# Kernel optimization log

Measured on AMD Instinct MI355X. Metric: run time of the kernel, lower is better.

## Reference

```python
import jax, jax.numpy as jnp
import numpy as np

B, S, P, H, W, TAG, M, K = 4, 2, 17, 128, 128, 1, 8, 10
PHW = P * H * W
SIGMA, SF = 0.2, 3.0
E_INV = float(np.e ** -1)
EPS = 1e-6


def setup_inputs() -> dict:
    key = jax.random.key(0)
    k1, k2, k3, k4, k5, k6, k7 = jax.random.split(key, 7)
    preds = jax.random.normal(k1, (B, S, (1 + TAG) * P, H, W), jnp.float32)
    gt_masks = jax.random.uniform(k2, (B, H, W), jnp.float32)
    gt_heatmaps = jax.random.uniform(k3, (B, P, H, W), jnp.float32)
    pos = jax.random.uniform(k4, (B, M, P, 2), jnp.float32) * H  # pixel coords
    vis = jax.random.randint(k5, (B, M, P, 1), 0, 2).astype(jnp.float32)
    gt_skeletons = jnp.concatenate([pos, vis], axis=-1)  # [B,M,P,3] = (x, y, vis)
    kp_idx = jax.random.randint(k6, (B, M, P, 1), 0, PHW)
    kp_vis = jax.random.randint(k7, (B, M, P, 1), 0, 2)
    gt_keypoints = jnp.concatenate([kp_idx, kp_vis], axis=-1).astype(jnp.int32)  # [B,M,J,2]
    return {"preds": preds, "gt_masks": gt_masks, "gt_heatmaps": gt_heatmaps,
            "gt_skeletons": gt_skeletons, "gt_keypoints": gt_keypoints}


def _clog(x):
    # torch BCE clamps log at -100
    return jnp.clip(jnp.log(x), -100.0, None)


def _tag_single(pt, kp):
    # pt: [TAG, PHW] tag map for one (image, stack); kp: [M, J, 2] int (flat_idx, vis)
    idx = kp[..., 0]
    vis = (kp[..., 1] > 0).astype(pt.dtype)  # [M, J]
    g = jnp.transpose(pt[:, idx], (1, 2, 0))  # [M, J, TAG]
    cnt = vis.sum(1)  # [M]
    valid = (cnt > 0).astype(pt.dtype)
    safe = jnp.maximum(cnt, 1.0)
    mean_tag = (g * vis[..., None]).sum(1) / safe[:, None]  # [M, TAG]
    # pull: per-person mean over (visible joints x tag dims) of squared deviation
    pull_pp = (((g - mean_tag[:, None]) ** 2) * vis[..., None]).sum((1, 2)) / (safe * TAG)
    num = valid.sum()
    pull = (pull_pp * valid).sum() / (num + EPS)
    d = ((mean_tag[:, None] - mean_tag[None]) ** 2).sum(-1)  # [M, M]
    pm = jnp.exp(-d) * valid[:, None] * valid[None]
    push = (pm.sum() - num) / ((num - 1.0) * num + EPS) * 0.5
    return push, pull


def _forward(preds, gt_masks, gt_heatmaps, gt_skeletons, gt_keypoints):
    hm = preds[:, :, :P]  # [B,S,P,H,W] raw heatmap logits
    prob = jax.nn.sigmoid(hm)
    # ---- detection loss (weighted BCE, per stack) ----
    t = (gt_heatmaps > E_INV).astype(jnp.float32)[:, None]  # [B,1,P,H,W]
    wgt = 10.0 * t + 0.5 * (gt_heatmaps < E_INV).astype(jnp.float32)[:, None]
    x = prob * gt_masks[:, None, None]
    bce = -(t * _clog(x) + (1.0 - t) * _clog(1.0 - x))
    det_loss = (wgt * bce).mean(axis=(0, 2, 3, 4))  # [S]
    # ---- associative embedding push/pull ----
    pred_tag_imgs = preds[:, :, P:(1 + TAG) * P].reshape(B, S, TAG, P, H, W)
    pred_tags = pred_tag_imgs.reshape(B, S, TAG, PHW)
    push, pull = jax.vmap(lambda ptb, kpb: jax.vmap(lambda pt: _tag_single(pt, kpb))(ptb))(
        pred_tags, gt_keypoints)  # each [B,S]
    # ---- keypoint sampling: top-K of flattened probability maps ----
    flat = prob.reshape(B, S, PHW)
    _, topi = jax.lax.top_k(flat, K)  # [B,S,K]
    part = topi // (H * W)
    rem = topi % (H * W)
    xi = rem // W
    yi = rem % W
    pos = jnp.stack([xi, yi], -1).astype(jnp.float32)  # [B,S,K,2]
    # ---- nearest-person matching (faithful to source, incl. vis==1 penalty) ----
    max_dist = float(H + W)
    sk_t = jnp.transpose(gt_skeletons, (0, 2, 1, 3))  # [B,P,M,3]
    pidx = jnp.broadcast_to(part.reshape(B, S * K)[:, :, None, None], (B, S * K, M, 3))
    sk_sel = jnp.take_along_axis(sk_t, pidx, axis=1).reshape(B, S, K, M, 3)
    vispen = max_dist * (sk_sel[..., 2] == 1).astype(jnp.float32)  # [B,S,K,M]
    dvec = vispen[..., None] + sk_sel[..., 1:] - pos[..., None, :]
    dist = jnp.sqrt((dvec ** 2).sum(-1) + 1e-12)
    person_ids = jnp.argmin(dist, axis=-1)  # [B,S,K]
    # ---- gather tag values at sampled locations ----
    pti = jnp.transpose(pred_tag_imgs, (0, 1, 3, 4, 5, 2))  # [B,S,P,H,W,TAG]
    bb = jnp.arange(B)[:, None, None]
    ss = jnp.arange(S)[None, :, None]
    tv = pti[bb, ss, part, xi, yi]  # [B,S,K,TAG]
    # ---- SkeletonGenerator: tag-conditioned soft-argmax ----
    aff = ((pti[:, :, None] - tv[:, :, :, None, None, None, :]) ** 2).sum(-1)  # [B,S,K,P,H,W]
    logits = SF * hm[:, :, None] - aff / (2.0 * SIGMA ** 2)
    wts = jax.nn.softmax(logits.reshape(B, S, K, P, H * W), -1).reshape(B, S, K, P, H, W)
    px = (wts * jnp.arange(H, dtype=jnp.float32)[:, None]).sum((-1, -2))  # [B,S,K,P]
    py = (wts * jnp.arange(W, dtype=jnp.float32)).sum((-1, -2))
    skel = jnp.stack([px, py], -1)  # [B,S,K,P,2]
    gts = gt_skeletons[bb, person_ids]  # [B,S,K,P,3]
    err = jnp.sqrt(((gts[..., :2] - skel) ** 2).sum(-1) + 1e-12) * (gts[..., 2] > 0)
    delta = 0.1
    a = jnp.abs(err)
    small = (a < delta).astype(jnp.float32)
    hub = small * err ** 2 + (1.0 - small) * delta * (a - delta / 2.0)
    skel_loss = hub.mean(-1).mean(-1)  # [B,S]
    # ---- weighted sum (loss_weights = (1,1,1,10)) ----
    return (1.0 * push.mean() + 1.0 * pull.mean() + 1.0 * det_loss.mean()
            + 10.0 * skel_loss.mean())


def reference(preds, gt_masks, gt_heatmaps, gt_skeletons, gt_keypoints):
    return _forward(preds, gt_masks, gt_heatmaps, gt_skeletons, gt_keypoints)
```

## Files before the change

### kernel.cpp

```cpp
#include <hip/hip_runtime.h>
#include <math.h>

#define B_ 4
#define S_ 2
#define P_ 17
#define H_ 128
#define W_ 128
#define M_ 8
#define K_ 10
#define HW_ (H_*W_)
#define PHW_ (P_*HW_)
#define CH_ 34
#define G_ 34
#define C_ 8192
#define E_INV_F 0.36787944117144233f
#define LOG2E 1.4426950408889634f
#define SF_ 3.0f
#define INV2SIG 12.5f
#define MAXDIST 256.0f

#define TOP1_BLOCKS (B_*S_*G_)
#define DET_BLOCKS  544
#define TAG_BLOCKS  (B_*S_)
#define MAIN_BLOCKS (TOP1_BLOCKS + DET_BLOCKS + TAG_BLOCKS)

#define SKEL_CHUNKS 4
#define NBSP (B_*S_*P_)
#define SKEL_BLOCKS (NBSP*SKEL_CHUNKS)

__device__ __forceinline__ unsigned int map32(float f) {
    unsigned int u = __float_as_uint(f);
    unsigned int flip = (unsigned int)((int)u >> 31) | 0x80000000u;
    return u ^ flip;
}

__device__ __forceinline__ void insert10(unsigned long long* a, unsigned long long key) {
    #pragma unroll
    for (int j = 9; j >= 1; --j) {
        unsigned long long am1 = a[j-1];
        a[j] = (key > am1) ? am1 : ((key > a[j]) ? key : a[j]);
    }
    a[0] = (key > a[0]) ? key : a[0];
}

__device__ __forceinline__ void merge10(unsigned long long* a, const unsigned long long* b) {
    #pragma unroll
    for (int t = 0; t < 10; ++t) {
        unsigned long long key = b[t];
        if (key > a[9]) insert10(a, key);
    }
}

__global__ __launch_bounds__(256, 4) void k_main(const float* __restrict__ preds,
                                                 const float* __restrict__ gmask,
                                                 const float* __restrict__ gh,
                                                 const int* __restrict__ kp,
                                                 unsigned long long* __restrict__ cand,
                                                 float* __restrict__ ws_det,
                                                 float* __restrict__ ws_tag) {
    int tid = threadIdx.x;
    if (blockIdx.x < TOP1_BLOCKS) {
        int bs = blockIdx.x / G_;
        int c  = blockIdx.x % G_;
        int wave = tid >> 6, lane = tid & 63;
        const float4* base = (const float4*)(preds + (size_t)bs*CH_*HW_ + (size_t)c*C_);
        unsigned long long a[10];
        #pragma unroll
        for (int j = 0; j < 10; ++j) a[j] = 0ull;
        for (int j = 0; j < 8; ++j) {
            int idx4 = wave*512 + j*64 + lane;
            float4 v = base[idx4];
            unsigned int i0 = (unsigned int)(c*C_ + idx4*4);
            const float* vv = &v.x;
            #pragma unroll
            for (int cc = 0; cc < 4; ++cc) {
                unsigned int key32 = map32(vv[cc]);
                unsigned int thr = (unsigned int)(a[9] >> 32);
                unsigned long long mask = __ballot(key32 >= thr);
                if (mask) {
                    unsigned long long kk =
                        ((unsigned long long)key32 << 32) | (unsigned int)(~(i0 + cc));
                    do {
                        int l = (int)__ffsll(mask) - 1;
                        unsigned long long cnd = __shfl(kk, l);
                        if (cnd > a[9]) insert10(a, cnd);
                        mask &= mask - 1;
                    } while (mask);
                }
            }
        }
        __shared__ unsigned long long smw[4][10];
        if (lane == 0) {
            #pragma unroll
            for (int j = 0; j < 10; ++j) smw[wave][j] = a[j];
        }
        __syncthreads();
        if (tid < 2) {
            unsigned long long x[10], y[10];
            #pragma unroll
            for (int j = 0; j < 10; ++j) { x[j] = smw[tid][j]; y[j] = smw[tid+2][j]; }
            merge10(x, y);
            #pragma unroll
            for (int j = 0; j < 10; ++j) smw[tid][j] = x[j];
        }
        __syncthreads();
        if (tid == 0) {
            unsigned long long x[10], y[10];
            #pragma unroll
            for (int j = 0; j < 10; ++j) { x[j] = smw[0][j]; y[j] = smw[1][j]; }
            merge10(x, y);
            #pragma unroll
            for (int j = 0; j < 10; ++j) cand[(size_t)blockIdx.x*10 + j] = x[j];
        }
    } else if (blockIdx.x < TOP1_BLOCKS + DET_BLOCKS) {
        int dblk = blockIdx.x - TOP1_BLOCKS;
        int t = dblk*256 + tid;
        float acc = 0.0f;
        #pragma unroll
        for (int j = 0; j < 4; ++j) {
            int q = t + j*(DET_BLOCKS*256);
            int hw4 = q & 4095;
            int t1  = q >> 12;
            int p   = t1 % P_;
            int t2  = t1 / P_;
            float4 hm4 = ((const float4*)preds)[(t2*CH_ + p)*4096 + hw4];
            float4 gm4 = ((const float4*)gmask)[(t2>>1)*4096 + hw4];
            float4 gh4 = ((const float4*)gh)[((t2>>1)*P_ + p)*4096 + hw4];
            const float* hmv = &hm4.x; const float* gmv = &gm4.x; const float* ghv4 = &gh4.x;
            #pragma unroll
            for (int cc = 0; cc < 4; ++cc) {
                float hm = hmv[cc];
                float e = exp2f(-fabsf(hm)*LOG2E);
                float r = __builtin_amdgcn_rcpf(1.0f + e);
                float prob = (hm >= 0.0f) ? r : e*r;
                float x = prob * gmv[cc];
                float ghv = ghv4[cc];
                float tt  = (ghv > E_INV_F) ? 1.0f : 0.0f;
                float wgt = 10.0f*tt + ((ghv < E_INV_F) ? 0.5f : 0.0f);
                float lx  = fmaxf(__logf(x),        -100.0f);
                float l1x = fmaxf(__logf(1.0f - x), -100.0f);
                acc += wgt * (-(tt*lx + (1.0f - tt)*l1x));
            }
        }
        #pragma unroll
        for (int off = 32; off > 0; off >>= 1) acc += __shfl_down(acc, off);
        __shared__ float sred[4];
        int wave = tid >> 6, lane = tid & 63;
        if (lane == 0) sred[wave] = acc;
        __syncthreads();
        if (tid == 0) ws_det[dblk] = sred[0] + sred[1] + sred[2] + sred[3];
    } else {
        int bs = blockIdx.x - (TOP1_BLOCKS + DET_BLOCKS);
        int b = bs / S_;
        __shared__ float g[M_*P_];
        __shared__ float vis[M_*P_];
        __shared__ float mean_tag[M_];
        __shared__ float validm[M_];
        __shared__ float pull_pp[M_];
        const float* tagbase = preds + ((size_t)bs*CH_ + P_)*HW_;
        if (tid < M_*P_) {
            int m = tid / P_; int p = tid % P_;
            int off = ((b*M_ + m)*P_ + p)*2;
            int idx = kp[off];
            int v   = kp[off+1];
            g[tid]   = tagbase[idx];
            vis[tid] = (v > 0) ? 1.0f : 0.0f;
        }
        __syncthreads();
        if (tid < M_) {
            float cnt = 0.0f, sum = 0.0f;
            for (int p = 0; p < P_; p++) { cnt += vis[tid*P_+p]; sum += g[tid*P_+p]*vis[tid*P_+p]; }
            float safe = fmaxf(cnt, 1.0f);
            float mt = sum / safe;
            mean_tag[tid] = mt;
            validm[tid] = (cnt > 0.0f) ? 1.0f : 0.0f;
            float pp = 0.0f;
            for (int p = 0; p < P_; p++) { float d = g[tid*P_+p] - mt; pp += d*d*vis[tid*P_+p]; }
            pull_pp[tid] = pp / safe;
        }
        __syncthreads();
        if (tid == 0) {
            float num = 0.0f;
            for (int m = 0; m < M_; m++) num += validm[m];
            float pull = 0.0f;
            for (int m = 0; m < M_; m++) pull += pull_pp[m]*validm[m];
            pull = pull / (num + 1e-6f);
            float pmsum = 0.0f;
            for (int i = 0; i < M_; i++)
                for (int j = 0; j < M_; j++) {
                    float d = mean_tag[i] - mean_tag[j]; d = d*d;
                    pmsum += expf(-d)*validm[i]*validm[j];
                }
            float push = (pmsum - num) / ((num - 1.0f)*num + 1e-6f) * 0.5f;
            ws_tag[bs] = push + pull;
        }
    }
}

__global__ __launch_bounds__(64) void k_top2(const float* __restrict__ preds,
                                             const float* __restrict__ gsk,
                                             const unsigned long long* __restrict__ cand,
                                             float* __restrict__ ws_tv,
                                             int* __restrict__ ws_pid) {
    int bs = blockIdx.x; int b = bs / S_;
    int tid = threadIdx.x;
    __shared__ unsigned long long sm[64*10];
    if (tid < G_) {
        #pragma unroll
        for (int j = 0; j < 10; ++j) sm[tid*10+j] = cand[((size_t)bs*G_ + tid)*10 + j];
    } else {
        #pragma unroll
        for (int j = 0; j < 10; ++j) sm[tid*10+j] = 0ull;
    }
    __syncthreads();
    for (int st = 32; st >= 1; st >>= 1) {
        if (tid < st) {
            unsigned long long x[10], y[10];
            #pragma unroll
            for (int j = 0; j < 10; ++j) { x[j] = sm[tid*10+j]; y[j] = sm[(tid+st)*10+j]; }
            merge10(x, y);
            #pragma unroll
            for (int j = 0; j < 10; ++j) sm[tid*10+j] = x[j];
        }
        __syncthreads();
    }
    if (tid < K_) {
        unsigned long long key = sm[tid];
        unsigned int topi = (unsigned int)(~key);
        int part = topi >> 14;
        int rem  = topi & (HW_-1);
        int xi   = rem >> 7;
        int yi   = rem & (W_-1);
        const float* tagbase = preds + ((size_t)bs*CH_ + P_)*HW_;
        float tv = tagbase[topi];
        float best = INFINITY; int pid = 0;
        for (int m = 0; m < M_; m++) {
            const float* sk = gsk + ((size_t)(b*M_ + m)*P_ + part)*3;
            float sk1 = sk[1], sk2 = sk[2];
            float vp = (sk2 == 1.0f) ? MAXDIST : 0.0f;
            float d0 = vp + sk1 - (float)xi;
            float d1 = vp + sk2 - (float)yi;
            float dist = sqrtf(d0*d0 + d1*d1 + 1e-12f);
            if (dist < best) { best = dist; pid = m; }
        }
        int o = bs*K_ + tid;
        ws_tv[o]  = tv;
        ws_pid[o] = pid;
    }
}

__global__ __launch_bounds__(256, 4) void k_skel(const float* __restrict__ preds,
                                                 const float* __restrict__ ws_tv,
                                                 float* __restrict__ ws_skl,
                                                 float* __restrict__ ws_ssx,
                                                 float* __restrict__ ws_ssy) {
    int bid   = blockIdx.x / SKEL_CHUNKS;
    int chunk = blockIdx.x % SKEL_CHUNKS;
    int p  = bid % P_;
    int bs = bid / P_;
    const float4* hm4 = (const float4*)(preds + ((size_t)bs*CH_ + p)*HW_);
    const float4* tg4 = (const float4*)(preds + ((size_t)bs*CH_ + P_ + p)*HW_);
    float tv[K_];
    #pragma unroll
    for (int k = 0; k < K_; k++) tv[k] = ws_tv[bs*K_ + k];
    float l[K_], sx[K_], sy[K_];
    #pragma unroll
    for (int k = 0; k < K_; k++) { l[k] = 0.0f; sx[k] = 0.0f; sy[k] = 0.0f; }
    int tid = threadIdx.x;
    const float C2 = INV2SIG * LOG2E;
    #pragma unroll
    for (int j = 0; j < 4; ++j) {
        int q = chunk*1024 + j*256 + tid;
        float4 hv = hm4[q];
        float4 tg = tg4[q];
        float h  = (float)(q >> 5);
        float w0 = (float)((q*4) & (W_-1));
        const float* hvv = &hv.x; const float* tgv = &tg.x;
        #pragma unroll
        for (int cc = 0; cc < 4; ++cc) {
            float a2 = (SF_*LOG2E) * hvv[cc];
            float tgc = tgv[cc];
            float w = w0 + (float)cc;
            #pragma unroll
            for (int k = 0; k < K_; k++) {
                float d = tgc - tv[k];
                float e = exp2f(fmaf(-C2, d*d, a2));
                l[k] += e;
                sx[k] = fmaf(e, h, sx[k]);
                sy[k] = fmaf(e, w, sy[k]);
            }
        }
    }
    #pragma unroll
    for (int k = 0; k < K_; k++) {
        for (int off = 32; off > 0; off >>= 1) {
            l[k]  += __shfl_down(l[k],  off);
            sx[k] += __shfl_down(sx[k], off);
            sy[k] += __shfl_down(sy[k], off);
        }
    }
    __shared__ float red[4][K_][3];
    int wave = tid >> 6, lane = tid & 63;
    if (lane == 0) {
        #pragma unroll
        for (int k = 0; k < K_; k++) {
            red[wave][k][0] = l[k]; red[wave][k][1] = sx[k]; red[wave][k][2] = sy[k];
        }
    }
    __syncthreads();
    if (tid < K_) {
        int k = tid;
        float L  = red[0][k][0] + red[1][k][0] + red[2][k][0] + red[3][k][0];
        float SX = red[0][k][1] + red[1][k][1] + red[2][k][1] + red[3][k][1];
        float SY = red[0][k][2] + red[1][k][2] + red[2][k][2] + red[3][k][2];
        int o = blockIdx.x*K_ + k;
        ws_skl[o] = L; ws_ssx[o] = SX; ws_ssy[o] = SY;
    }
}

__global__ __launch_bounds__(256) void k_fin(const float* __restrict__ gsk,
                                             const int* __restrict__ ws_pid,
                                             const float* __restrict__ ws_skl,
                                             const float* __restrict__ ws_ssx,
                                             const float* __restrict__ ws_ssy,
                                             const float* __restrict__ ws_det,
                                             const float* __restrict__ ws_tag,
                                             float* __restrict__ out) {
    int tid = threadIdx.x;
    float acc = 0.0f;
    for (int i = tid; i < DET_BLOCKS; i += 256) acc += ws_det[i];
    acc *= (1.0f/(float)(B_*S_*P_*HW_));
    if (tid < B_*S_) acc += ws_tag[tid] * (1.0f/(float)(B_*S_));
    for (int idx = tid; idx < NBSP*K_; idx += 256) {
        int bid = idx / K_;
        int k   = idx % K_;
        int p  = bid % P_;
        int bs = bid / P_;
        int b  = bs / S_;
        float L = 0.0f, SX = 0.0f, SY = 0.0f;
        #pragma unroll
        for (int c = 0; c < SKEL_CHUNKS; ++c) {
            int o = (bid*SKEL_CHUNKS + c)*K_ + k;
            L += ws_skl[o]; SX += ws_ssx[o]; SY += ws_ssy[o];
        }
        float px = SX / L, py = SY / L;
        int pid = ws_pid[bs*K_ + k];
        const float* g = gsk + ((size_t)(b*M_ + pid)*P_ + p)*3;
        float d0 = g[0] - px, d1 = g[1] - py;
        float gate = (g[2] > 0.0f) ? 1.0f : 0.0f;
        float err = sqrtf(d0*d0 + d1*d1 + 1e-12f) * gate;
        float hub = (err < 0.1f) ? err*err : 0.1f*(err - 0.05f);
        acc += hub * (10.0f/(float)(B_*S_*K_*P_));
    }
    #pragma unroll
    for (int off = 32; off > 0; off >>= 1) acc += __shfl_down(acc, off);
    __shared__ float sred[4];
    int wave = tid >> 6, lane = tid & 63;
    if (lane == 0) sred[wave] = acc;
    __syncthreads();
    if (tid == 0) out[0] = sred[0] + sred[1] + sred[2] + sred[3];
}

extern "C" void kernel_launch(void* const* d_in, const int* in_sizes, int n_in,
                              void* d_out, int out_size, void* d_ws, size_t ws_size,
                              hipStream_t stream) {
    (void)in_sizes; (void)n_in; (void)out_size; (void)ws_size;
    const float* preds = (const float*)d_in[0];
    const float* gmask = (const float*)d_in[1];
    const float* gh    = (const float*)d_in[2];
    const float* gsk   = (const float*)d_in[3];
    const int*   gkp   = (const int*)d_in[4];
    float* out = (float*)d_out;
    unsigned long long* cand = (unsigned long long*)d_ws;
    float* ws_tv  = (float*)(cand + (size_t)B_*S_*G_*10);
    int*   ws_pid = (int*)(ws_tv + (size_t)B_*S_*K_);
    float* ws_skl = (float*)(ws_pid + (size_t)B_*S_*K_);
    float* ws_ssx = ws_skl + (size_t)SKEL_BLOCKS*K_;
    float* ws_ssy = ws_ssx + (size_t)SKEL_BLOCKS*K_;
    float* ws_det = ws_ssy + (size_t)SKEL_BLOCKS*K_;
    float* ws_tag = ws_det + DET_BLOCKS;

    hipLaunchKernelGGL(k_main, dim3(MAIN_BLOCKS), dim3(256), 0, stream,
                       preds, gmask, gh, gkp, cand, ws_det, ws_tag);
    hipLaunchKernelGGL(k_top2, dim3(B_*S_),       dim3(64),  0, stream,
                       preds, gsk, cand, ws_tv, ws_pid);
    hipLaunchKernelGGL(k_skel, dim3(SKEL_BLOCKS), dim3(256), 0, stream,
                       preds, ws_tv, ws_skl, ws_ssx, ws_ssy);
    hipLaunchKernelGGL(k_fin,  dim3(1),           dim3(256), 0, stream,
                       gsk, ws_pid, ws_skl, ws_ssx, ws_ssy, ws_det, ws_tag, out);
}
```

Baseline: 129.6 us.

## Fuse detection BCE into top-k scan and merge top2 into skeleton kernel

The detection-loss pass now runs inside the top-k scan blocks, so each heatmap element is read once for both the candidate search and the BCE. The separate k_top2 launch is removed: every k_skel block redoes the candidate merge and tag lookup in shared memory, and one block per (b,s) writes the person ids. This saves a launch and a second read of the heatmap channels. The cost is redundant merge work repeated across 272 skeleton blocks and heavier per-element work in the scan loop.

```diff
diff --git a/kernel.cpp b/kernel.cpp
--- a/kernel.cpp
+++ b/kernel.cpp
@@ -19,10 +19,8 @@
 #define INV2SIG 12.5f
 #define MAXDIST 256.0f
 
-#define TOP1_BLOCKS (B_*S_*G_)
-#define DET_BLOCKS  544
-#define TAG_BLOCKS  (B_*S_)
-#define MAIN_BLOCKS (TOP1_BLOCKS + DET_BLOCKS + TAG_BLOCKS)
+#define SCAN_BLOCKS (B_*S_*G_)
+#define MAIN_BLOCKS (SCAN_BLOCKS + B_*S_)
 
 #define SKEL_CHUNKS 4
 #define NBSP (B_*S_*P_)
@@ -51,30 +49,49 @@
     }
 }
 
-__global__ __launch_bounds__(256, 4) void k_main(const float* __restrict__ preds,
-                                                 const float* __restrict__ gmask,
-                                                 const float* __restrict__ gh,
-                                                 const int* __restrict__ kp,
-                                                 unsigned long long* __restrict__ cand,
-                                                 float* __restrict__ ws_det,
-                                                 float* __restrict__ ws_tag) {
+__global__ __launch_bounds__(256) void k_main(const float* __restrict__ preds,
+                                              const float* __restrict__ gmask,
+                                              const float* __restrict__ gh,
+                                              const int* __restrict__ kp,
+                                              unsigned long long* __restrict__ cand,
+                                              float* __restrict__ ws_det,
+                                              float* __restrict__ ws_tag) {
     int tid = threadIdx.x;
-    if (blockIdx.x < TOP1_BLOCKS) {
+    if (blockIdx.x < SCAN_BLOCKS) {
         int bs = blockIdx.x / G_;
         int c  = blockIdx.x % G_;
+        int p    = c >> 1;
+        int half = c & 1;
+        int b    = bs / S_;
         int wave = tid >> 6, lane = tid & 63;
         const float4* base = (const float4*)(preds + (size_t)bs*CH_*HW_ + (size_t)c*C_);
+        const float4* gm4p = (const float4*)gmask + (size_t)b*4096 + half*2048;
+        const float4* gh4p = (const float4*)gh + ((size_t)b*P_ + p)*4096 + half*2048;
         unsigned long long a[10];
         #pragma unroll
         for (int j = 0; j < 10; ++j) a[j] = 0ull;
+        float det_acc = 0.0f;
         for (int j = 0; j < 8; ++j) {
             int idx4 = wave*512 + j*64 + lane;
-            float4 v = base[idx4];
+            float4 v  = base[idx4];
+            float4 gm = gm4p[idx4];
+            float4 gv = gh4p[idx4];
             unsigned int i0 = (unsigned int)(c*C_ + idx4*4);
-            const float* vv = &v.x;
+            const float* vv = &v.x; const float* gmv = &gm.x; const float* ghv4 = &gv.x;
             #pragma unroll
             for (int cc = 0; cc < 4; ++cc) {
-                unsigned int key32 = map32(vv[cc]);
+                float hm = vv[cc];
+                float e = exp2f(-fabsf(hm)*LOG2E);
+                float r = __builtin_amdgcn_rcpf(1.0f + e);
+                float prob = (hm >= 0.0f) ? r : e*r;
+                float x = prob * gmv[cc];
+                float ghv = ghv4[cc];
+                float tt  = (ghv > E_INV_F) ? 1.0f : 0.0f;
+                float wgt = 10.0f*tt + ((ghv < E_INV_F) ? 0.5f : 0.0f);
+                float lx  = fmaxf(__logf(x),        -100.0f);
+                float l1x = fmaxf(__logf(1.0f - x), -100.0f);
+                det_acc += wgt * (-(tt*lx + (1.0f - tt)*l1x));
+                unsigned int key32 = map32(hm);
                 unsigned int thr = (unsigned int)(a[9] >> 32);
                 unsigned long long mask = __ballot(key32 >= thr);
                 if (mask) {
@@ -89,12 +106,17 @@
                 }
             }
         }
+        #pragma unroll
+        for (int off = 32; off > 0; off >>= 1) det_acc += __shfl_down(det_acc, off);
+        __shared__ float sred[4];
         __shared__ unsigned long long smw[4][10];
         if (lane == 0) {
+            sred[wave] = det_acc;
             #pragma unroll
             for (int j = 0; j < 10; ++j) smw[wave][j] = a[j];
         }
         __syncthreads();
+        if (tid == 0) ws_det[blockIdx.x] = sred[0] + sred[1] + sred[2] + sred[3];
         if (tid < 2) {
             unsigned long long x[10], y[10];
             #pragma unroll
@@ -112,45 +134,8 @@
             #pragma unroll
             for (int j = 0; j < 10; ++j) cand[(size_t)blockIdx.x*10 + j] = x[j];
         }
-    } else if (blockIdx.x < TOP1_BLOCKS + DET_BLOCKS) {
-        int dblk = blockIdx.x - TOP1_BLOCKS;
-        int t = dblk*256 + tid;
-        float acc = 0.0f;
-        #pragma unroll
-        for (int j = 0; j < 4; ++j) {
-            int q = t + j*(DET_BLOCKS*256);
-            int hw4 = q & 4095;
-            int t1  = q >> 12;
-            int p   = t1 % P_;
-            int t2  = t1 / P_;
-            float4 hm4 = ((const float4*)preds)[(t2*CH_ + p)*4096 + hw4];
-            float4 gm4 = ((const float4*)gmask)[(t2>>1)*4096 + hw4];
-            float4 gh4 = ((const float4*)gh)[((t2>>1)*P_ + p)*4096 + hw4];
-            const float* hmv = &hm4.x; const float* gmv = &gm4.x; const float* ghv4 = &gh4.x;
-            #pragma unroll
-            for (int cc = 0; cc < 4; ++cc) {
-                float hm = hmv[cc];
-                float e = exp2f(-fabsf(hm)*LOG2E);
-                float r = __builtin_amdgcn_rcpf(1.0f + e);
-                float prob = (hm >= 0.0f) ? r : e*r;
-                float x = prob * gmv[cc];
-                float ghv = ghv4[cc];
-                float tt  = (ghv > E_INV_F) ? 1.0f : 0.0f;
-                float wgt = 10.0f*tt + ((ghv < E_INV_F) ? 0.5f : 0.0f);
-                float lx  = fmaxf(__logf(x),        -100.0f);
-                float l1x = fmaxf(__logf(1.0f - x), -100.0f);
-                acc += wgt * (-(tt*lx + (1.0f - tt)*l1x));
-            }
-        }
-        #pragma unroll
-        for (int off = 32; off > 0; off >>= 1) acc += __shfl_down(acc, off);
-        __shared__ float sred[4];
-        int wave = tid >> 6, lane = tid & 63;
-        if (lane == 0) sred[wave] = acc;
-        __syncthreads();
-        if (tid == 0) ws_det[dblk] = sred[0] + sred[1] + sred[2] + sred[3];
     } else {
-        int bs = blockIdx.x - (TOP1_BLOCKS + DET_BLOCKS);
+        int bs = blockIdx.x - SCAN_BLOCKS;
         int b = bs / S_;
         __shared__ float g[M_*P_];
         __shared__ float vis[M_*P_];
@@ -161,10 +146,8 @@
         if (tid < M_*P_) {
             int m = tid / P_; int p = tid % P_;
             int off = ((b*M_ + m)*P_ + p)*2;
-            int idx = kp[off];
-            int v   = kp[off+1];
-            g[tid]   = tagbase[idx];
-            vis[tid] = (v > 0) ? 1.0f : 0.0f;
+            g[tid]   = tagbase[kp[off]];
+            vis[tid] = (kp[off+1] > 0) ? 1.0f : 0.0f;
         }
         __syncthreads();
         if (tid < M_) {
@@ -197,60 +180,10 @@
     }
 }
 
-__global__ __launch_bounds__(64) void k_top2(const float* __restrict__ preds,
-                                             const float* __restrict__ gsk,
-                                             const unsigned long long* __restrict__ cand,
-                                             float* __restrict__ ws_tv,
-                                             int* __restrict__ ws_pid) {
-    int bs = blockIdx.x; int b = bs / S_;
-    int tid = threadIdx.x;
-    __shared__ unsigned long long sm[64*10];
-    if (tid < G_) {
-        #pragma unroll
-        for (int j = 0; j < 10; ++j) sm[tid*10+j] = cand[((size_t)bs*G_ + tid)*10 + j];
-    } else {
-        #pragma unroll
-        for (int j = 0; j < 10; ++j) sm[tid*10+j] = 0ull;
-    }
-    __syncthreads();
-    for (int st = 32; st >= 1; st >>= 1) {
-        if (tid < st) {
-            unsigned long long x[10], y[10];
-            #pragma unroll
-            for (int j = 0; j < 10; ++j) { x[j] = sm[tid*10+j]; y[j] = sm[(tid+st)*10+j]; }
-            merge10(x, y);
-            #pragma unroll
-            for (int j = 0; j < 10; ++j) sm[tid*10+j] = x[j];
-        }
-        __syncthreads();
-    }
-    if (tid < K_) {
-        unsigned long long key = sm[tid];
-        unsigned int topi = (unsigned int)(~key);
-        int part = topi >> 14;
-        int rem  = topi & (HW_-1);
-        int xi   = rem >> 7;
-        int yi   = rem & (W_-1);
-        const float* tagbase = preds + ((size_t)bs*CH_ + P_)*HW_;
-        float tv = tagbase[topi];
-        float best = INFINITY; int pid = 0;
-        for (int m = 0; m < M_; m++) {
-            const float* sk = gsk + ((size_t)(b*M_ + m)*P_ + part)*3;
-            float sk1 = sk[1], sk2 = sk[2];
-            float vp = (sk2 == 1.0f) ? MAXDIST : 0.0f;
-            float d0 = vp + sk1 - (float)xi;
-            float d1 = vp + sk2 - (float)yi;
-            float dist = sqrtf(d0*d0 + d1*d1 + 1e-12f);
-            if (dist < best) { best = dist; pid = m; }
-        }
-        int o = bs*K_ + tid;
-        ws_tv[o]  = tv;
-        ws_pid[o] = pid;
-    }
-}
-
 __global__ __launch_bounds__(256, 4) void k_skel(const float* __restrict__ preds,
-                                                 const float* __restrict__ ws_tv,
+                                                 const float* __restrict__ gsk,
+                                                 const unsigned long long* __restrict__ cand,
+                                                 int* __restrict__ ws_pid,
                                                  float* __restrict__ ws_skl,
                                                  float* __restrict__ ws_ssx,
                                                  float* __restrict__ ws_ssy) {
@@ -258,15 +191,64 @@
     int chunk = blockIdx.x % SKEL_CHUNKS;
     int p  = bid % P_;
     int bs = bid / P_;
+    int b  = bs / S_;
+    int tid = threadIdx.x;
+    const float* tagbase = preds + ((size_t)bs*CH_ + P_)*HW_;
+
+    __shared__ unsigned long long sm[64*10];
+    __shared__ float stv[K_];
+    if (tid < 64) {
+        if (tid < G_) {
+            #pragma unroll
+            for (int j = 0; j < 10; ++j) sm[tid*10+j] = cand[((size_t)bs*G_ + tid)*10 + j];
+        } else {
+            #pragma unroll
+            for (int j = 0; j < 10; ++j) sm[tid*10+j] = 0ull;
+        }
+    }
+    __syncthreads();
+    for (int st = 32; st >= 1; st >>= 1) {
+        if (tid < st) {
+            unsigned long long x[10], y[10];
+            #pragma unroll
+            for (int j = 0; j < 10; ++j) { x[j] = sm[tid*10+j]; y[j] = sm[(tid+st)*10+j]; }
+            merge10(x, y);
+            #pragma unroll
+            for (int j = 0; j < 10; ++j) sm[tid*10+j] = x[j];
+        }
+        __syncthreads();
+    }
+    if (tid < K_) {
+        unsigned int topi = (unsigned int)(~sm[tid]);
+        stv[tid] = tagbase[topi];
+        if (p == 0 && chunk == 0) {
+            int part = topi >> 14;
+            int rem  = topi & (HW_-1);
+            int xi   = rem >> 7;
+            int yi   = rem & (W_-1);
+            float best = INFINITY; int pid = 0;
+            for (int m = 0; m < M_; m++) {
+                const float* sk = gsk + ((size_t)(b*M_ + m)*P_ + part)*3;
+                float sk1 = sk[1], sk2 = sk[2];
+                float vp = (sk2 == 1.0f) ? MAXDIST : 0.0f;
+                float d0 = vp + sk1 - (float)xi;
+                float d1 = vp + sk2 - (float)yi;
+                float dist = sqrtf(d0*d0 + d1*d1 + 1e-12f);
+                if (dist < best) { best = dist; pid = m; }
+            }
+            ws_pid[bs*K_ + tid] = pid;
+        }
+    }
+    __syncthreads();
+
     const float4* hm4 = (const float4*)(preds + ((size_t)bs*CH_ + p)*HW_);
-    const float4* tg4 = (const float4*)(preds + ((size_t)bs*CH_ + P_ + p)*HW_);
+    const float4* tg4 = (const float4*)(tagbase + (size_t)p*HW_);
     float tv[K_];
     #pragma unroll
-    for (int k = 0; k < K_; k++) tv[k] = ws_tv[bs*K_ + k];
+    for (int k = 0; k < K_; k++) tv[k] = stv[k];
     float l[K_], sx[K_], sy[K_];
     #pragma unroll
     for (int k = 0; k < K_; k++) { l[k] = 0.0f; sx[k] = 0.0f; sy[k] = 0.0f; }
-    int tid = threadIdx.x;
     const float C2 = INV2SIG * LOG2E;
     #pragma unroll
     for (int j = 0; j < 4; ++j) {
@@ -328,7 +310,7 @@
                                              float* __restrict__ out) {
     int tid = threadIdx.x;
     float acc = 0.0f;
-    for (int i = tid; i < DET_BLOCKS; i += 256) acc += ws_det[i];
+    for (int i = tid; i < SCAN_BLOCKS; i += 256) acc += ws_det[i];
     acc *= (1.0f/(float)(B_*S_*P_*HW_));
     if (tid < B_*S_) acc += ws_tag[tid] * (1.0f/(float)(B_*S_));
     for (int idx = tid; idx < NBSP*K_; idx += 256) {
@@ -372,20 +354,17 @@
     const int*   gkp   = (const int*)d_in[4];
     float* out = (float*)d_out;
     unsigned long long* cand = (unsigned long long*)d_ws;
-    float* ws_tv  = (float*)(cand + (size_t)B_*S_*G_*10);
-    int*   ws_pid = (int*)(ws_tv + (size_t)B_*S_*K_);
+    int*   ws_pid = (int*)(cand + (size_t)SCAN_BLOCKS*10);
     float* ws_skl = (float*)(ws_pid + (size_t)B_*S_*K_);
     float* ws_ssx = ws_skl + (size_t)SKEL_BLOCKS*K_;
     float* ws_ssy = ws_ssx + (size_t)SKEL_BLOCKS*K_;
     float* ws_det = ws_ssy + (size_t)SKEL_BLOCKS*K_;
-    float* ws_tag = ws_det + DET_BLOCKS;
+    float* ws_tag = ws_det + SCAN_BLOCKS;
 
     hipLaunchKernelGGL(k_main, dim3(MAIN_BLOCKS), dim3(256), 0, stream,
                        preds, gmask, gh, gkp, cand, ws_det, ws_tag);
-    hipLaunchKernelGGL(k_top2, dim3(B_*S_),       dim3(64),  0, stream,
-                       preds, gsk, cand, ws_tv, ws_pid);
     hipLaunchKernelGGL(k_skel, dim3(SKEL_BLOCKS), dim3(256), 0, stream,
-                       preds, ws_tv, ws_skl, ws_ssx, ws_ssy);
+                       preds, gsk, cand, ws_pid, ws_skl, ws_ssx, ws_ssy);
     hipLaunchKernelGGL(k_fin,  dim3(1),           dim3(256), 0, stream,
                        gsk, ws_pid, ws_skl, ws_ssx, ws_ssy, ws_det, ws_tag, out);
 }
```

Result: slower. 135.3 us (+4.4%).
